# Kernel optimization log

Hardware: AMD Instinct MI355X
Metric: run time of the kernel (lower is better)

## Reference

```python
import jax, jax.numpy as jnp
import numpy as np

TOPK = 2


def setup_inputs() -> dict:
    key = jax.random.key(0)
    k0, k1, k2, k3, k4 = jax.random.split(key, 5)
    B, S, D, E, H = 4, 2048, 1024, 8, 2816
    return {
        "x": jax.random.normal(k0, (B, S, D), dtype=jnp.float32),
        "gate_w": jax.random.normal(k1, (E, D), dtype=jnp.float32) * 0.02,
        "w1": jax.random.normal(k2, (E, H, D), dtype=jnp.float32) * 0.02,
        "w2": jax.random.normal(k3, (E, D, H), dtype=jnp.float32) * 0.02,
        "w3": jax.random.normal(k4, (E, H, D), dtype=jnp.float32) * 0.02,
    }


def reference(x, gate_w, w1, w2, w3):
    B, S, D = x.shape
    E = gate_w.shape[0]
    T = B * S
    xf = x.reshape(T, D)

    # Router: top-k logits, softmax over the selected k, scatter into a
    # dense [T, E] combine-weight matrix (equivalent to the index_add combine).
    logits = xf @ gate_w.T                      # [T, E]
    tw, ti = jax.lax.top_k(logits, TOPK)        # [T, k]
    tw = jax.nn.softmax(tw, axis=-1)
    cw = jnp.zeros((T, E), dtype=xf.dtype).at[
        jnp.arange(T)[:, None], ti
    ].add(tw)                                   # [T, E] combine weights

    # Expert SwiGLU FFNs, combined with routing weights. Loop over the small
    # fixed expert count; tokens with cw==0 contribute zero, matching the
    # masked dispatch in the original module.
    out = jnp.zeros_like(xf)
    for e in range(E):
        h = jax.nn.silu(xf @ w1[e].T) * (xf @ w3[e].T)   # [T, H]
        out = out + cw[:, e:e + 1] * (h @ w2[e].T)       # [T, D]
    return out.reshape(B, S, D)
```

## Files before the change

### kernel.cpp

```cpp
#include <hip/hip_runtime.h>
#include <stdint.h>

#define T_TOK 8192
#define DIM   1024
#define NEXP  8
#define HID   2816

typedef __bf16 bf16x8 __attribute__((ext_vector_type(8)));
typedef float  f32x4  __attribute__((ext_vector_type(4)));

typedef __attribute__((address_space(3))) uint32_t lds_u32_t;
typedef __attribute__((address_space(1))) const uint32_t gbl_u32_t;

__device__ __forceinline__ void gl_lds16(const void* g, void* l) {
    __builtin_amdgcn_global_load_lds((gbl_u32_t*)g, (lds_u32_t*)l, 16, 0, 0);
}

__device__ __forceinline__ uint32_t f2bf_u(float f) {
    uint32_t u = __builtin_bit_cast(uint32_t, f);
    return u + 0x7fffu + ((u >> 16) & 1u);
}
__device__ __forceinline__ uint32_t pack2(float a, float b) {
    return (f2bf_u(a) >> 16) | (f2bf_u(b) & 0xffff0000u);
}


__global__ __launch_bounds__(256) void cvt_k(
    const float* __restrict__ s, unsigned short* __restrict__ d, int n8)
{
    int i = blockIdx.x * 256 + threadIdx.x;
    if (i < n8) {
        const float4* sp = (const float4*)(s + (size_t)i * 8);
        float4 a = sp[0], b = sp[1];
        uint4 o;
        o.x = pack2(a.x, a.y); o.y = pack2(a.z, a.w);
        o.z = pack2(b.x, b.y); o.w = pack2(b.z, b.w);
        ((uint4*)d)[i] = o;
    }
}

__global__ __launch_bounds__(256) void router_k(
    const float* __restrict__ x, const float* __restrict__ gw,
    int* __restrict__ cnt, int* __restrict__ slot_list,
    float* __restrict__ slot_w)
{
    const int wave = threadIdx.x >> 6, lane = threadIdx.x & 63;
    const int t = blockIdx.x * 4 + wave;
    const float4* xp = (const float4*)(x + (size_t)t * DIM + lane * 16);
    float4 xv[4];
#pragma unroll
    for (int i = 0; i < 4; ++i) xv[i] = xp[i];

    double lg[NEXP];
#pragma unroll
    for (int e = 0; e < NEXP; ++e) {
        const float4* gp = (const float4*)(gw + (size_t)e * DIM + lane * 16);
        double s = 0.0;
#pragma unroll
        for (int i = 0; i < 4; ++i) {
            float4 g = gp[i];
            s += (double)xv[i].x * g.x + (double)xv[i].y * g.y +
                 (double)xv[i].z * g.z + (double)xv[i].w * g.w;
        }
#pragma unroll
        for (int m = 32; m >= 1; m >>= 1) s += __shfl_xor(s, m, 64);
        lg[e] = s;
    }

    if (lane == 0) {
        int e0 = 0; double b0 = lg[0];
#pragma unroll
        for (int e = 1; e < NEXP; ++e)
            if (lg[e] > b0) { b0 = lg[e]; e0 = e; }
        int e1 = -1; double b1 = -1.0e300;
#pragma unroll
        for (int e = 0; e < NEXP; ++e)
            if (e != e0 && lg[e] > b1) { b1 = lg[e]; e1 = e; }

        float p0 = (float)(1.0 / (1.0 + exp(b1 - b0)));
        float p1 = 1.0f - p0;

        int pos0 = atomicAdd(&cnt[e0], 1);
        slot_list[e0 * T_TOK + pos0] = 2 * t;
        slot_w[2 * t] = p0;
        int pos1 = atomicAdd(&cnt[e1], 1);
        slot_list[e1 * T_TOK + pos1] = 2 * t + 1;
        slot_w[2 * t + 1] = p1;
    }
}

__global__ __launch_bounds__(256) void ffn1_k(
    const unsigned short* __restrict__ xb, const unsigned short* __restrict__ w1b,
    const unsigned short* __restrict__ w3b, const int* __restrict__ cnt,
    const int* __restrict__ slot_list, unsigned short* __restrict__ h_ws)
{
    __shared__ unsigned short As[128 * 32];
    __shared__ unsigned short B1s[64 * 32];
    __shared__ unsigned short B2s[64 * 32];
    __shared__ int slots_s[128];

    const int e = blockIdx.z;
    const int cntE = cnt[e];
    const int m0 = blockIdx.y * 128;
    if (m0 >= cntE) return;
    const int n0 = blockIdx.x * 64;
    const int tid = threadIdx.x;
    const int wave = tid >> 6, lane = tid & 63;

    if (tid < 128) {
        int idx = m0 + tid;
        slots_s[tid] = (idx < cntE) ? slot_list[e * T_TOK + idx] : -1;
    }
    __syncthreads();

    const int rr = lane >> 2;
    const int qsw = (lane & 3) ^ ((rr >> 1) & 3);
    const unsigned short* gsrc[4];
    unsigned short* ldst[4];
    if (wave < 2) {
#pragma unroll
        for (int i = 0; i < 4; ++i) {
            int row = wave * 64 + i * 16 + rr;
            int slot = slots_s[row];
            int tok = (slot >= 0) ? (slot >> 1) : 0;
            gsrc[i] = xb + (size_t)tok * DIM + qsw * 8;
            ldst[i] = &As[(wave * 64 + i * 16) * 32];
        }
    } else if (wave == 2) {
#pragma unroll
        for (int i = 0; i < 4; ++i) {
            int row = i * 16 + rr;
            gsrc[i] = w1b + ((size_t)e * HID + n0 + row) * DIM + qsw * 8;
            ldst[i] = &B1s[(i * 16) * 32];
        }
    } else {
#pragma unroll
        for (int i = 0; i < 4; ++i) {
            int row = i * 16 + rr;
            gsrc[i] = w3b + ((size_t)e * HID + n0 + row) * DIM + qsw * 8;
            ldst[i] = &B2s[(i * 16) * 32];
        }
    }

    const int wm = wave >> 1, wn = wave & 1;
    const int lrow = lane & 15, quad = lane >> 4;
    const int ksw = (quad ^ ((lrow >> 1) & 3)) * 8;

    f32x4 acc1[4][2], acc2[4][2];
    const f32x4 zf = {0.f, 0.f, 0.f, 0.f};
#pragma unroll
    for (int mi = 0; mi < 4; ++mi)
#pragma unroll
        for (int ni = 0; ni < 2; ++ni) { acc1[mi][ni] = zf; acc2[mi][ni] = zf; }

    for (int k0 = 0; k0 < DIM; k0 += 32) {
#pragma unroll
        for (int i = 0; i < 4; ++i) gl_lds16(gsrc[i], ldst[i]);
#pragma unroll
        for (int i = 0; i < 4; ++i) gsrc[i] += 32;
        __syncthreads();

        bf16x8 af[4], b1f[2], b2f[2];
#pragma unroll
        for (int mi = 0; mi < 4; ++mi)
            af[mi] = *(const bf16x8*)&As[(wm * 64 + mi * 16 + lrow) * 32 + ksw];
#pragma unroll
        for (int ni = 0; ni < 2; ++ni) {
            b1f[ni] = *(const bf16x8*)&B1s[(wn * 32 + ni * 16 + lrow) * 32 + ksw];
            b2f[ni] = *(const bf16x8*)&B2s[(wn * 32 + ni * 16 + lrow) * 32 + ksw];
        }
#pragma unroll
        for (int mi = 0; mi < 4; ++mi)
#pragma unroll
            for (int ni = 0; ni < 2; ++ni) {
                acc1[mi][ni] = __builtin_amdgcn_mfma_f32_16x16x32_bf16(
                    af[mi], b1f[ni], acc1[mi][ni], 0, 0, 0);
                acc2[mi][ni] = __builtin_amdgcn_mfma_f32_16x16x32_bf16(
                    af[mi], b2f[ni], acc2[mi][ni], 0, 0, 0);
            }
        __syncthreads();
    }

#pragma unroll
    for (int mi = 0; mi < 4; ++mi) {
#pragma unroll
        for (int r = 0; r < 4; ++r) {
            int mloc = wm * 64 + mi * 16 + quad * 4 + r;
            int slot = slots_s[mloc];
            if (slot >= 0) {
                unsigned short* hrow =
                    h_ws + (size_t)slot * HID + n0 + wn * 32 + lrow;
#pragma unroll
                for (int ni = 0; ni < 2; ++ni) {
                    float a1 = acc1[mi][ni][r], a3 = acc2[mi][ni][r];
                    float hv = (a1 / (1.f + __expf(-a1))) * a3;
                    hrow[ni * 16] = (unsigned short)(f2bf_u(hv) >> 16);
                }
            }
        }
    }
}

__global__ __launch_bounds__(256) void ffn2_k(
    const unsigned short* __restrict__ h_ws, const unsigned short* __restrict__ w2b,
    const int* __restrict__ cnt, const int* __restrict__ slot_list,
    const float* __restrict__ slot_w, float* __restrict__ out)
{
    __shared__ unsigned short As[128 * 32];
    __shared__ unsigned short Bs[128 * 32];
    __shared__ int slots_s[128];
    __shared__ float wgt_s[128];

    const int e = blockIdx.z;
    const int cntE = cnt[e];
    const int m0 = blockIdx.y * 128;
    if (m0 >= cntE) return;
    const int n0 = blockIdx.x * 128;
    const int tid = threadIdx.x;
    const int wave = tid >> 6, lane = tid & 63;

    if (tid < 128) {
        int idx = m0 + tid;
        int s = (idx < cntE) ? slot_list[e * T_TOK + idx] : -1;
        slots_s[tid] = s;
        wgt_s[tid] = (s >= 0) ? slot_w[s] : 0.f;
    }
    __syncthreads();

    const int rr = lane >> 2;
    const int qsw = (lane & 3) ^ ((rr >> 1) & 3);
    const unsigned short* gsrc[4];
    unsigned short* ldst[4];
    if (wave < 2) {
#pragma unroll
        for (int i = 0; i < 4; ++i) {
            int row = wave * 64 + i * 16 + rr;
            int slot = slots_s[row];
            int s = (slot >= 0) ? slot : 0;
            gsrc[i] = h_ws + (size_t)s * HID + qsw * 8;
            ldst[i] = &As[(wave * 64 + i * 16) * 32];
        }
    } else {
#pragma unroll
        for (int i = 0; i < 4; ++i) {
            int row = (wave - 2) * 64 + i * 16 + rr;
            gsrc[i] = w2b + ((size_t)e * DIM + n0 + row) * HID + qsw * 8;
            ldst[i] = &Bs[((wave - 2) * 64 + i * 16) * 32];
        }
    }

    const int wm = wave >> 1, wn = wave & 1;
    const int lrow = lane & 15, quad = lane >> 4;
    const int ksw = (quad ^ ((lrow >> 1) & 3)) * 8;

    f32x4 acc[4][4];
    const f32x4 zf = {0.f, 0.f, 0.f, 0.f};
#pragma unroll
    for (int mi = 0; mi < 4; ++mi)
#pragma unroll
        for (int ni = 0; ni < 4; ++ni) acc[mi][ni] = zf;

    for (int k0 = 0; k0 < HID; k0 += 32) {
#pragma unroll
        for (int i = 0; i < 4; ++i) gl_lds16(gsrc[i], ldst[i]);
#pragma unroll
        for (int i = 0; i < 4; ++i) gsrc[i] += 32;
        __syncthreads();

        bf16x8 af[4], bf[4];
#pragma unroll
        for (int mi = 0; mi < 4; ++mi)
            af[mi] = *(const bf16x8*)&As[(wm * 64 + mi * 16 + lrow) * 32 + ksw];
#pragma unroll
        for (int ni = 0; ni < 4; ++ni)
            bf[ni] = *(const bf16x8*)&Bs[(wn * 64 + ni * 16 + lrow) * 32 + ksw];
#pragma unroll
        for (int mi = 0; mi < 4; ++mi)
#pragma unroll
            for (int ni = 0; ni < 4; ++ni)
                acc[mi][ni] = __builtin_amdgcn_mfma_f32_16x16x32_bf16(
                    af[mi], bf[ni], acc[mi][ni], 0, 0, 0);
        __syncthreads();
    }

#pragma unroll
    for (int mi = 0; mi < 4; ++mi) {
#pragma unroll
        for (int r = 0; r < 4; ++r) {
            int mloc = wm * 64 + mi * 16 + quad * 4 + r;
            int slot = slots_s[mloc];
            if (slot >= 0) {
                int tok = slot >> 1;
                float w = wgt_s[mloc];
                float* orow = out + (size_t)tok * DIM + n0 + wn * 64 + lrow;
#pragma unroll
                for (int ni = 0; ni < 4; ++ni)
                    atomicAdd(&orow[ni * 16], acc[mi][ni][r] * w);
            }
        }
    }
}

extern "C" void kernel_launch(void* const* d_in, const int* in_sizes, int n_in,
                              void* d_out, int out_size, void* d_ws, size_t ws_size,
                              hipStream_t stream) {
    const float* x  = (const float*)d_in[0];
    const float* gw = (const float*)d_in[1];
    const float* w1 = (const float*)d_in[2];
    const float* w2 = (const float*)d_in[3];
    const float* w3 = (const float*)d_in[4];
    float* out = (float*)d_out;

    char* ws = (char*)d_ws;
    int*   cnt       = (int*)ws;
    int*   slot_list = (int*)(ws + 256);
    float* slot_w    = (float*)(ws + 256 + NEXP * T_TOK * 4);
    unsigned short* h_ws = (unsigned short*)(ws + 327936);
    unsigned short* x_bf = (unsigned short*)(ws + 92602624);
    unsigned short* w1_bf = (unsigned short*)(ws + 109379840);
    unsigned short* w3_bf = (unsigned short*)(ws + 155517184);
    unsigned short* w2_bf = (unsigned short*)(ws + 201654528);

    hipMemsetAsync(cnt, 0, 256, stream);
    hipMemsetAsync(out, 0, (size_t)T_TOK * DIM * sizeof(float), stream);

    const int nx = T_TOK * DIM / 8;
    const int nw = NEXP * HID * DIM / 8;
    cvt_k<<<(nx + 255) / 256, 256, 0, stream>>>(x, x_bf, nx);
    cvt_k<<<(nw + 255) / 256, 256, 0, stream>>>(w1, w1_bf, nw);
    cvt_k<<<(nw + 255) / 256, 256, 0, stream>>>(w3, w3_bf, nw);
    cvt_k<<<(nw + 255) / 256, 256, 0, stream>>>(w2, w2_bf, nw);

    router_k<<<T_TOK / 4, 256, 0, stream>>>(x, gw, cnt, slot_list, slot_w);
    ffn1_k<<<dim3(HID / 64, T_TOK / 128, NEXP), 256, 0, stream>>>(
        x_bf, w1_bf, w3_bf, cnt, slot_list, h_ws);
    ffn2_k<<<dim3(DIM / 128, T_TOK / 128, NEXP), 256, 0, stream>>>(
        h_ws, w2_bf, cnt, slot_list, slot_w, out);
}
```

Before: 929.4 us.

## Double-buffer LDS tiles in both expert GEMM kernels and raise MFMA priority

Both expert GEMM kernels (ffn1 and ffn2) now keep two LDS buffers per operand. Each iteration issues the global-to-LDS loads for the next K slice before running the MFMAs on the current slice, so memory latency overlaps with compute and only one barrier is needed per iteration instead of two. The MFMA block is also wrapped in s_setprio to favour issuing matrix instructions. The cost is double the LDS footprint per block, which may lower occupancy.

```diff
diff --git a/kernel.cpp b/kernel.cpp
--- a/kernel.cpp
+++ b/kernel.cpp
@@ -94,9 +94,9 @@
     const unsigned short* __restrict__ w3b, const int* __restrict__ cnt,
     const int* __restrict__ slot_list, unsigned short* __restrict__ h_ws)
 {
-    __shared__ unsigned short As[128 * 32];
-    __shared__ unsigned short B1s[64 * 32];
-    __shared__ unsigned short B2s[64 * 32];
+    __shared__ unsigned short As[2][128 * 32];
+    __shared__ unsigned short B1s[2][64 * 32];
+    __shared__ unsigned short B2s[2][64 * 32];
     __shared__ int slots_s[128];
 
     const int e = blockIdx.z;
@@ -117,28 +117,32 @@
     const int qsw = (lane & 3) ^ ((rr >> 1) & 3);
     const unsigned short* gsrc[4];
     unsigned short* ldst[4];
+    int bstride;
     if (wave < 2) {
+        bstride = 128 * 32;
 #pragma unroll
         for (int i = 0; i < 4; ++i) {
             int row = wave * 64 + i * 16 + rr;
             int slot = slots_s[row];
             int tok = (slot >= 0) ? (slot >> 1) : 0;
             gsrc[i] = xb + (size_t)tok * DIM + qsw * 8;
-            ldst[i] = &As[(wave * 64 + i * 16) * 32];
+            ldst[i] = &As[0][(wave * 64 + i * 16) * 32];
         }
     } else if (wave == 2) {
+        bstride = 64 * 32;
 #pragma unroll
         for (int i = 0; i < 4; ++i) {
             int row = i * 16 + rr;
             gsrc[i] = w1b + ((size_t)e * HID + n0 + row) * DIM + qsw * 8;
-            ldst[i] = &B1s[(i * 16) * 32];
+            ldst[i] = &B1s[0][(i * 16) * 32];
         }
     } else {
+        bstride = 64 * 32;
 #pragma unroll
         for (int i = 0; i < 4; ++i) {
             int row = i * 16 + rr;
             gsrc[i] = w3b + ((size_t)e * HID + n0 + row) * DIM + qsw * 8;
-            ldst[i] = &B2s[(i * 16) * 32];
+            ldst[i] = &B2s[0][(i * 16) * 32];
         }
     }
 
@@ -153,22 +157,36 @@
 #pragma unroll
         for (int ni = 0; ni < 2; ++ni) { acc1[mi][ni] = zf; acc2[mi][ni] = zf; }
 
-    for (int k0 = 0; k0 < DIM; k0 += 32) {
-#pragma unroll
-        for (int i = 0; i < 4; ++i) gl_lds16(gsrc[i], ldst[i]);
-#pragma unroll
-        for (int i = 0; i < 4; ++i) gsrc[i] += 32;
-        __syncthreads();
+    const int NST = DIM / 32;
+#pragma unroll
+    for (int i = 0; i < 4; ++i) gl_lds16(gsrc[i], ldst[i]);
+#pragma unroll
+    for (int i = 0; i < 4; ++i) gsrc[i] += 32;
+    __syncthreads();
+
+    for (int t = 0; t < NST; ++t) {
+        const int cur = t & 1, nxt = cur ^ 1;
+        if (t + 1 < NST) {
+#pragma unroll
+            for (int i = 0; i < 4; ++i)
+                gl_lds16(gsrc[i], ldst[i] + nxt * bstride);
+#pragma unroll
+            for (int i = 0; i < 4; ++i) gsrc[i] += 32;
+        }
+        const unsigned short* Ab  = &As[cur][0];
+        const unsigned short* B1b = &B1s[cur][0];
+        const unsigned short* B2b = &B2s[cur][0];
 
         bf16x8 af[4], b1f[2], b2f[2];
 #pragma unroll
         for (int mi = 0; mi < 4; ++mi)
-            af[mi] = *(const bf16x8*)&As[(wm * 64 + mi * 16 + lrow) * 32 + ksw];
+            af[mi] = *(const bf16x8*)&Ab[(wm * 64 + mi * 16 + lrow) * 32 + ksw];
 #pragma unroll
         for (int ni = 0; ni < 2; ++ni) {
-            b1f[ni] = *(const bf16x8*)&B1s[(wn * 32 + ni * 16 + lrow) * 32 + ksw];
-            b2f[ni] = *(const bf16x8*)&B2s[(wn * 32 + ni * 16 + lrow) * 32 + ksw];
-        }
+            b1f[ni] = *(const bf16x8*)&B1b[(wn * 32 + ni * 16 + lrow) * 32 + ksw];
+            b2f[ni] = *(const bf16x8*)&B2b[(wn * 32 + ni * 16 + lrow) * 32 + ksw];
+        }
+        __builtin_amdgcn_s_setprio(1);
 #pragma unroll
         for (int mi = 0; mi < 4; ++mi)
 #pragma unroll
@@ -178,7 +196,9 @@
                 acc2[mi][ni] = __builtin_amdgcn_mfma_f32_16x16x32_bf16(
                     af[mi], b2f[ni], acc2[mi][ni], 0, 0, 0);
             }
-        __syncthreads();
+        __builtin_amdgcn_s_setprio(0);
+
+        if (t + 1 < NST) __syncthreads();
     }
 
 #pragma unroll
@@ -206,8 +226,8 @@
     const int* __restrict__ cnt, const int* __restrict__ slot_list,
     const float* __restrict__ slot_w, float* __restrict__ out)
 {
-    __shared__ unsigned short As[128 * 32];
-    __shared__ unsigned short Bs[128 * 32];
+    __shared__ unsigned short As[2][128 * 32];
+    __shared__ unsigned short Bs[2][128 * 32];
     __shared__ int slots_s[128];
     __shared__ float wgt_s[128];
 
@@ -231,6 +251,7 @@
     const int qsw = (lane & 3) ^ ((rr >> 1) & 3);
     const unsigned short* gsrc[4];
     unsigned short* ldst[4];
+    const int bstride = 128 * 32;
     if (wave < 2) {
 #pragma unroll
         for (int i = 0; i < 4; ++i) {
@@ -238,14 +259,14 @@
             int slot = slots_s[row];
             int s = (slot >= 0) ? slot : 0;
             gsrc[i] = h_ws + (size_t)s * HID + qsw * 8;
-            ldst[i] = &As[(wave * 64 + i * 16) * 32];
+            ldst[i] = &As[0][(wave * 64 + i * 16) * 32];
         }
     } else {
 #pragma unroll
         for (int i = 0; i < 4; ++i) {
             int row = (wave - 2) * 64 + i * 16 + rr;
             gsrc[i] = w2b + ((size_t)e * DIM + n0 + row) * HID + qsw * 8;
-            ldst[i] = &Bs[((wave - 2) * 64 + i * 16) * 32];
+            ldst[i] = &Bs[0][((wave - 2) * 64 + i * 16) * 32];
         }
     }
 
@@ -260,27 +281,42 @@
 #pragma unroll
         for (int ni = 0; ni < 4; ++ni) acc[mi][ni] = zf;
 
-    for (int k0 = 0; k0 < HID; k0 += 32) {
-#pragma unroll
-        for (int i = 0; i < 4; ++i) gl_lds16(gsrc[i], ldst[i]);
-#pragma unroll
-        for (int i = 0; i < 4; ++i) gsrc[i] += 32;
-        __syncthreads();
+    const int NST = HID / 32;
+#pragma unroll
+    for (int i = 0; i < 4; ++i) gl_lds16(gsrc[i], ldst[i]);
+#pragma unroll
+    for (int i = 0; i < 4; ++i) gsrc[i] += 32;
+    __syncthreads();
+
+    for (int t = 0; t < NST; ++t) {
+        const int cur = t & 1, nxt = cur ^ 1;
+        if (t + 1 < NST) {
+#pragma unroll
+            for (int i = 0; i < 4; ++i)
+                gl_lds16(gsrc[i], ldst[i] + nxt * bstride);
+#pragma unroll
+            for (int i = 0; i < 4; ++i) gsrc[i] += 32;
+        }
+        const unsigned short* Ab = &As[cur][0];
+        const unsigned short* Bb = &Bs[cur][0];
 
         bf16x8 af[4], bf[4];
 #pragma unroll
         for (int mi = 0; mi < 4; ++mi)
-            af[mi] = *(const bf16x8*)&As[(wm * 64 + mi * 16 + lrow) * 32 + ksw];
+            af[mi] = *(const bf16x8*)&Ab[(wm * 64 + mi * 16 + lrow) * 32 + ksw];
 #pragma unroll
         for (int ni = 0; ni < 4; ++ni)
-            bf[ni] = *(const bf16x8*)&Bs[(wn * 64 + ni * 16 + lrow) * 32 + ksw];
+            bf[ni] = *(const bf16x8*)&Bb[(wn * 64 + ni * 16 + lrow) * 32 + ksw];
+        __builtin_amdgcn_s_setprio(1);
 #pragma unroll
         for (int mi = 0; mi < 4; ++mi)
 #pragma unroll
             for (int ni = 0; ni < 4; ++ni)
                 acc[mi][ni] = __builtin_amdgcn_mfma_f32_16x16x32_bf16(
                     af[mi], bf[ni], acc[mi][ni], 0, 0, 0);
-        __syncthreads();
+        __builtin_amdgcn_s_setprio(0);
+
+        if (t + 1 < NST) __syncthreads();
     }
 
 #pragma unroll
```

After: 941.0 us. No clear change (+1.2%).

## Double-buffer activation tiles in LDS and load weights directly into registers

Applied to the files above, without the earlier changes.

Both expert GEMM kernels now stage only the gathered activation rows in LDS, using a two-stage ping-pong buffer. Weight fragments are loaded straight from global memory into registers, also double-buffered, so the next K-step loads overlap the current MFMAs, and s_setprio is raised around the MFMA bursts. This aims to hide global load latency and drop one of the two barriers per K-step. In exchange, each wave fetches its own weight fragments with no reuse across the waves that share the same columns, which uses more registers and global bandwidth.

```diff
diff --git a/kernel.cpp b/kernel.cpp
--- a/kernel.cpp
+++ b/kernel.cpp
@@ -94,9 +94,7 @@
     const unsigned short* __restrict__ w3b, const int* __restrict__ cnt,
     const int* __restrict__ slot_list, unsigned short* __restrict__ h_ws)
 {
-    __shared__ unsigned short As[128 * 32];
-    __shared__ unsigned short B1s[64 * 32];
-    __shared__ unsigned short B2s[64 * 32];
+    __shared__ unsigned short As[2][128 * 32];
     __shared__ int slots_s[128];
 
     const int e = blockIdx.z;
@@ -115,37 +113,27 @@
 
     const int rr = lane >> 2;
     const int qsw = (lane & 3) ^ ((rr >> 1) & 3);
-    const unsigned short* gsrc[4];
-    unsigned short* ldst[4];
-    if (wave < 2) {
-#pragma unroll
-        for (int i = 0; i < 4; ++i) {
-            int row = wave * 64 + i * 16 + rr;
-            int slot = slots_s[row];
-            int tok = (slot >= 0) ? (slot >> 1) : 0;
-            gsrc[i] = xb + (size_t)tok * DIM + qsw * 8;
-            ldst[i] = &As[(wave * 64 + i * 16) * 32];
-        }
-    } else if (wave == 2) {
-#pragma unroll
-        for (int i = 0; i < 4; ++i) {
-            int row = i * 16 + rr;
-            gsrc[i] = w1b + ((size_t)e * HID + n0 + row) * DIM + qsw * 8;
-            ldst[i] = &B1s[(i * 16) * 32];
-        }
-    } else {
-#pragma unroll
-        for (int i = 0; i < 4; ++i) {
-            int row = i * 16 + rr;
-            gsrc[i] = w3b + ((size_t)e * HID + n0 + row) * DIM + qsw * 8;
-            ldst[i] = &B2s[(i * 16) * 32];
-        }
+    const unsigned short* gsrc[2];
+    unsigned short* ldst[2];
+    const int bstride = 128 * 32;
+#pragma unroll
+    for (int i = 0; i < 2; ++i) {
+        int row = wave * 32 + i * 16 + rr;
+        int slot = slots_s[row];
+        int tok = (slot >= 0) ? (slot >> 1) : 0;
+        gsrc[i] = xb + (size_t)tok * DIM + qsw * 8;
+        ldst[i] = &As[0][(wave * 32 + i * 16) * 32];
     }
 
     const int wm = wave >> 1, wn = wave & 1;
     const int lrow = lane & 15, quad = lane >> 4;
     const int ksw = (quad ^ ((lrow >> 1) & 3)) * 8;
 
+    const unsigned short* w1p =
+        w1b + ((size_t)e * HID + n0 + wn * 32 + lrow) * DIM + quad * 8;
+    const unsigned short* w3p =
+        w3b + ((size_t)e * HID + n0 + wn * 32 + lrow) * DIM + quad * 8;
+
     f32x4 acc1[4][2], acc2[4][2];
     const f32x4 zf = {0.f, 0.f, 0.f, 0.f};
 #pragma unroll
@@ -153,32 +141,85 @@
 #pragma unroll
         for (int ni = 0; ni < 2; ++ni) { acc1[mi][ni] = zf; acc2[mi][ni] = zf; }
 
-    for (int k0 = 0; k0 < DIM; k0 += 32) {
-#pragma unroll
-        for (int i = 0; i < 4; ++i) gl_lds16(gsrc[i], ldst[i]);
-#pragma unroll
-        for (int i = 0; i < 4; ++i) gsrc[i] += 32;
-        __syncthreads();
-
-        bf16x8 af[4], b1f[2], b2f[2];
-#pragma unroll
-        for (int mi = 0; mi < 4; ++mi)
-            af[mi] = *(const bf16x8*)&As[(wm * 64 + mi * 16 + lrow) * 32 + ksw];
-#pragma unroll
-        for (int ni = 0; ni < 2; ++ni) {
-            b1f[ni] = *(const bf16x8*)&B1s[(wn * 32 + ni * 16 + lrow) * 32 + ksw];
-            b2f[ni] = *(const bf16x8*)&B2s[(wn * 32 + ni * 16 + lrow) * 32 + ksw];
-        }
-#pragma unroll
-        for (int mi = 0; mi < 4; ++mi)
-#pragma unroll
-            for (int ni = 0; ni < 2; ++ni) {
-                acc1[mi][ni] = __builtin_amdgcn_mfma_f32_16x16x32_bf16(
-                    af[mi], b1f[ni], acc1[mi][ni], 0, 0, 0);
-                acc2[mi][ni] = __builtin_amdgcn_mfma_f32_16x16x32_bf16(
-                    af[mi], b2f[ni], acc2[mi][ni], 0, 0, 0);
-            }
-        __syncthreads();
+    const int NST = DIM / 32;
+
+    bf16x8 bA10, bA11, bA30, bA31;
+    bf16x8 bB10, bB11, bB30, bB31;
+
+#pragma unroll
+    for (int i = 0; i < 2; ++i) { gl_lds16(gsrc[i], ldst[i]); gsrc[i] += 32; }
+    bA10 = *(const bf16x8*)(w1p);
+    bA11 = *(const bf16x8*)(w1p + 16 * DIM);
+    bA30 = *(const bf16x8*)(w3p);
+    bA31 = *(const bf16x8*)(w3p + 16 * DIM);
+    w1p += 32; w3p += 32;
+    __syncthreads();
+
+    for (int t = 0; t < NST; t += 2) {
+        {
+#pragma unroll
+            for (int i = 0; i < 2; ++i) {
+                gl_lds16(gsrc[i], ldst[i] + bstride); gsrc[i] += 32;
+            }
+            bB10 = *(const bf16x8*)(w1p);
+            bB11 = *(const bf16x8*)(w1p + 16 * DIM);
+            bB30 = *(const bf16x8*)(w3p);
+            bB31 = *(const bf16x8*)(w3p + 16 * DIM);
+            w1p += 32; w3p += 32;
+
+            const unsigned short* Ab = &As[0][0];
+            bf16x8 af[4];
+#pragma unroll
+            for (int mi = 0; mi < 4; ++mi)
+                af[mi] = *(const bf16x8*)&Ab[(wm * 64 + mi * 16 + lrow) * 32 + ksw];
+            __builtin_amdgcn_s_setprio(1);
+#pragma unroll
+            for (int mi = 0; mi < 4; ++mi) {
+                acc1[mi][0] = __builtin_amdgcn_mfma_f32_16x16x32_bf16(
+                    af[mi], bA10, acc1[mi][0], 0, 0, 0);
+                acc1[mi][1] = __builtin_amdgcn_mfma_f32_16x16x32_bf16(
+                    af[mi], bA11, acc1[mi][1], 0, 0, 0);
+                acc2[mi][0] = __builtin_amdgcn_mfma_f32_16x16x32_bf16(
+                    af[mi], bA30, acc2[mi][0], 0, 0, 0);
+                acc2[mi][1] = __builtin_amdgcn_mfma_f32_16x16x32_bf16(
+                    af[mi], bA31, acc2[mi][1], 0, 0, 0);
+            }
+            __builtin_amdgcn_s_setprio(0);
+            __syncthreads();
+        }
+        {
+            const bool more = (t + 2 < NST);
+            if (more) {
+#pragma unroll
+                for (int i = 0; i < 2; ++i) {
+                    gl_lds16(gsrc[i], ldst[i]); gsrc[i] += 32;
+                }
+                bA10 = *(const bf16x8*)(w1p);
+                bA11 = *(const bf16x8*)(w1p + 16 * DIM);
+                bA30 = *(const bf16x8*)(w3p);
+                bA31 = *(const bf16x8*)(w3p + 16 * DIM);
+                w1p += 32; w3p += 32;
+            }
+            const unsigned short* Ab = &As[1][0];
+            bf16x8 af[4];
+#pragma unroll
+            for (int mi = 0; mi < 4; ++mi)
+                af[mi] = *(const bf16x8*)&Ab[(wm * 64 + mi * 16 + lrow) * 32 + ksw];
+            __builtin_amdgcn_s_setprio(1);
+#pragma unroll
+            for (int mi = 0; mi < 4; ++mi) {
+                acc1[mi][0] = __builtin_amdgcn_mfma_f32_16x16x32_bf16(
+                    af[mi], bB10, acc1[mi][0], 0, 0, 0);
+                acc1[mi][1] = __builtin_amdgcn_mfma_f32_16x16x32_bf16(
+                    af[mi], bB11, acc1[mi][1], 0, 0, 0);
+                acc2[mi][0] = __builtin_amdgcn_mfma_f32_16x16x32_bf16(
+                    af[mi], bB30, acc2[mi][0], 0, 0, 0);
+                acc2[mi][1] = __builtin_amdgcn_mfma_f32_16x16x32_bf16(
+                    af[mi], bB31, acc2[mi][1], 0, 0, 0);
+            }
+            __builtin_amdgcn_s_setprio(0);
+            if (more) __syncthreads();
+        }
     }
 
 #pragma unroll
@@ -206,8 +247,7 @@
     const int* __restrict__ cnt, const int* __restrict__ slot_list,
     const float* __restrict__ slot_w, float* __restrict__ out)
 {
-    __shared__ unsigned short As[128 * 32];
-    __shared__ unsigned short Bs[128 * 32];
+    __shared__ unsigned short As[2][128 * 32];
     __shared__ int slots_s[128];
     __shared__ float wgt_s[128];
 
@@ -229,30 +269,25 @@
 
     const int rr = lane >> 2;
     const int qsw = (lane & 3) ^ ((rr >> 1) & 3);
-    const unsigned short* gsrc[4];
-    unsigned short* ldst[4];
-    if (wave < 2) {
-#pragma unroll
-        for (int i = 0; i < 4; ++i) {
-            int row = wave * 64 + i * 16 + rr;
-            int slot = slots_s[row];
-            int s = (slot >= 0) ? slot : 0;
-            gsrc[i] = h_ws + (size_t)s * HID + qsw * 8;
-            ldst[i] = &As[(wave * 64 + i * 16) * 32];
-        }
-    } else {
-#pragma unroll
-        for (int i = 0; i < 4; ++i) {
-            int row = (wave - 2) * 64 + i * 16 + rr;
-            gsrc[i] = w2b + ((size_t)e * DIM + n0 + row) * HID + qsw * 8;
-            ldst[i] = &Bs[((wave - 2) * 64 + i * 16) * 32];
-        }
+    const unsigned short* gsrc[2];
+    unsigned short* ldst[2];
+    const int bstride = 128 * 32;
+#pragma unroll
+    for (int i = 0; i < 2; ++i) {
+        int row = wave * 32 + i * 16 + rr;
+        int slot = slots_s[row];
+        int s = (slot >= 0) ? slot : 0;
+        gsrc[i] = h_ws + (size_t)s * HID + qsw * 8;
+        ldst[i] = &As[0][(wave * 32 + i * 16) * 32];
     }
 
     const int wm = wave >> 1, wn = wave & 1;
     const int lrow = lane & 15, quad = lane >> 4;
     const int ksw = (quad ^ ((lrow >> 1) & 3)) * 8;
 
+    const unsigned short* w2p =
+        w2b + ((size_t)e * DIM + n0 + wn * 64 + lrow) * HID + quad * 8;
+
     f32x4 acc[4][4];
     const f32x4 zf = {0.f, 0.f, 0.f, 0.f};
 #pragma unroll
@@ -260,27 +295,85 @@
 #pragma unroll
         for (int ni = 0; ni < 4; ++ni) acc[mi][ni] = zf;
 
-    for (int k0 = 0; k0 < HID; k0 += 32) {
-#pragma unroll
-        for (int i = 0; i < 4; ++i) gl_lds16(gsrc[i], ldst[i]);
-#pragma unroll
-        for (int i = 0; i < 4; ++i) gsrc[i] += 32;
-        __syncthreads();
-
-        bf16x8 af[4], bf[4];
-#pragma unroll
-        for (int mi = 0; mi < 4; ++mi)
-            af[mi] = *(const bf16x8*)&As[(wm * 64 + mi * 16 + lrow) * 32 + ksw];
-#pragma unroll
-        for (int ni = 0; ni < 4; ++ni)
-            bf[ni] = *(const bf16x8*)&Bs[(wn * 64 + ni * 16 + lrow) * 32 + ksw];
-#pragma unroll
-        for (int mi = 0; mi < 4; ++mi)
-#pragma unroll
-            for (int ni = 0; ni < 4; ++ni)
-                acc[mi][ni] = __builtin_amdgcn_mfma_f32_16x16x32_bf16(
-                    af[mi], bf[ni], acc[mi][ni], 0, 0, 0);
-        __syncthreads();
+    const int NST = HID / 32;
+
+    bf16x8 bA0, bA1, bA2, bA3;
+    bf16x8 bB0, bB1, bB2, bB3;
+
+#pragma unroll
+    for (int i = 0; i < 2; ++i) { gl_lds16(gsrc[i], ldst[i]); gsrc[i] += 32; }
+    bA0 = *(const bf16x8*)(w2p);
+    bA1 = *(const bf16x8*)(w2p + 16 * HID);
+    bA2 = *(const bf16x8*)(w2p + 32 * HID);
+    bA3 = *(const bf16x8*)(w2p + 48 * HID);
+    w2p += 32;
+    __syncthreads();
+
+    for (int t = 0; t < NST; t += 2) {
+        {
+#pragma unroll
+            for (int i = 0; i < 2; ++i) {
+                gl_lds16(gsrc[i], ldst[i] + bstride); gsrc[i] += 32;
+            }
+            bB0 = *(const bf16x8*)(w2p);
+            bB1 = *(const bf16x8*)(w2p + 16 * HID);
+            bB2 = *(const bf16x8*)(w2p + 32 * HID);
+            bB3 = *(const bf16x8*)(w2p + 48 * HID);
+            w2p += 32;
+
+            const unsigned short* Ab = &As[0][0];
+            bf16x8 af[4];
+#pragma unroll
+            for (int mi = 0; mi < 4; ++mi)
+                af[mi] = *(const bf16x8*)&Ab[(wm * 64 + mi * 16 + lrow) * 32 + ksw];
+            __builtin_amdgcn_s_setprio(1);
+#pragma unroll
+            for (int mi = 0; mi < 4; ++mi) {
+                acc[mi][0] = __builtin_amdgcn_mfma_f32_16x16x32_bf16(
+                    af[mi], bA0, acc[mi][0], 0, 0, 0);
+                acc[mi][1] = __builtin_amdgcn_mfma_f32_16x16x32_bf16(
+                    af[mi], bA1, acc[mi][1], 0, 0, 0);
+                acc[mi][2] = __builtin_amdgcn_mfma_f32_16x16x32_bf16(
+                    af[mi], bA2, acc[mi][2], 0, 0, 0);
+                acc[mi][3] = __builtin_amdgcn_mfma_f32_16x16x32_bf16(
+                    af[mi], bA3, acc[mi][3], 0, 0, 0);
+            }
+            __builtin_amdgcn_s_setprio(0);
+            __syncthreads();
+        }
+        {
+            const bool more = (t + 2 < NST);
+            if (more) {
+#pragma unroll
+                for (int i = 0; i < 2; ++i) {
+                    gl_lds16(gsrc[i], ldst[i]); gsrc[i] += 32;
+                }
+                bA0 = *(const bf16x8*)(w2p);
+                bA1 = *(const bf16x8*)(w2p + 16 * HID);
+                bA2 = *(const bf16x8*)(w2p + 32 * HID);
+                bA3 = *(const bf16x8*)(w2p + 48 * HID);
+                w2p += 32;
+            }
+            const unsigned short* Ab = &As[1][0];
+            bf16x8 af[4];
+#pragma unroll
+            for (int mi = 0; mi < 4; ++mi)
+                af[mi] = *(const bf16x8*)&Ab[(wm * 64 + mi * 16 + lrow) * 32 + ksw];
+            __builtin_amdgcn_s_setprio(1);
+#pragma unroll
+            for (int mi = 0; mi < 4; ++mi) {
+                acc[mi][0] = __builtin_amdgcn_mfma_f32_16x16x32_bf16(
+                    af[mi], bB0, acc[mi][0], 0, 0, 0);
+                acc[mi][1] = __builtin_amdgcn_mfma_f32_16x16x32_bf16(
+                    af[mi], bB1, acc[mi][1], 0, 0, 0);
+                acc[mi][2] = __builtin_amdgcn_mfma_f32_16x16x32_bf16(
+                    af[mi], bB2, acc[mi][2], 0, 0, 0);
+                acc[mi][3] = __builtin_amdgcn_mfma_f32_16x16x32_bf16(
+                    af[mi], bB3, acc[mi][3], 0, 0, 0);
+            }
+            __builtin_amdgcn_s_setprio(0);
+            if (more) __syncthreads();
+        }
     }
 
 #pragma unroll
```

New measurement: 1.301 ms. 1.4x slower.

## Triple-buffer FFN GEMM loads and replace atomic combine with per-slot output pass

Applied to the files above, without the earlier changes.

Both expert GEMM kernels now use a three-stage LDS ring with async global-to-LDS loads, a partial vmcnt wait plus one barrier per step, and raised wave priority around the MFMA block, so memory loads overlap compute. The second GEMM writes weighted per-slot results to a workspace instead of doing atomic adds into the output. A new combine kernel sums each token's two slots, which also drops the output memset. This costs triple LDS per block, which may lower occupancy, and adds an extra pass over a large fp32 buffer that reuses the x_bf workspace region after it is consumed.

```diff
diff --git a/kernel.cpp b/kernel.cpp
--- a/kernel.cpp
+++ b/kernel.cpp
@@ -24,6 +24,11 @@
     return (f2bf_u(a) >> 16) | (f2bf_u(b) & 0xffff0000u);
 }
 
+
+#define WAIT4 do { asm volatile("s_waitcnt vmcnt(4)" ::: "memory"); \
+    __builtin_amdgcn_s_barrier(); __builtin_amdgcn_sched_barrier(0); } while (0)
+#define WAIT0 do { asm volatile("s_waitcnt vmcnt(0)" ::: "memory"); \
+    __builtin_amdgcn_s_barrier(); __builtin_amdgcn_sched_barrier(0); } while (0)
 
 __global__ __launch_bounds__(256) void cvt_k(
     const float* __restrict__ s, unsigned short* __restrict__ d, int n8)
@@ -94,9 +99,9 @@
     const unsigned short* __restrict__ w3b, const int* __restrict__ cnt,
     const int* __restrict__ slot_list, unsigned short* __restrict__ h_ws)
 {
-    __shared__ unsigned short As[128 * 32];
-    __shared__ unsigned short B1s[64 * 32];
-    __shared__ unsigned short B2s[64 * 32];
+    __shared__ unsigned short As[3][128 * 32];
+    __shared__ unsigned short B1s[3][64 * 32];
+    __shared__ unsigned short B2s[3][64 * 32];
     __shared__ int slots_s[128];
 
     const int e = blockIdx.z;
@@ -116,7 +121,7 @@
     const int rr = lane >> 2;
     const int qsw = (lane & 3) ^ ((rr >> 1) & 3);
     const unsigned short* gsrc[4];
-    unsigned short* ldst[4];
+    unsigned short *l0[4], *l1[4], *l2[4];
     if (wave < 2) {
 #pragma unroll
         for (int i = 0; i < 4; ++i) {
@@ -124,21 +129,27 @@
             int slot = slots_s[row];
             int tok = (slot >= 0) ? (slot >> 1) : 0;
             gsrc[i] = xb + (size_t)tok * DIM + qsw * 8;
-            ldst[i] = &As[(wave * 64 + i * 16) * 32];
+            l0[i] = &As[0][(wave * 64 + i * 16) * 32];
+            l1[i] = &As[1][(wave * 64 + i * 16) * 32];
+            l2[i] = &As[2][(wave * 64 + i * 16) * 32];
         }
     } else if (wave == 2) {
 #pragma unroll
         for (int i = 0; i < 4; ++i) {
             int row = i * 16 + rr;
             gsrc[i] = w1b + ((size_t)e * HID + n0 + row) * DIM + qsw * 8;
-            ldst[i] = &B1s[(i * 16) * 32];
+            l0[i] = &B1s[0][(i * 16) * 32];
+            l1[i] = &B1s[1][(i * 16) * 32];
+            l2[i] = &B1s[2][(i * 16) * 32];
         }
     } else {
 #pragma unroll
         for (int i = 0; i < 4; ++i) {
             int row = i * 16 + rr;
             gsrc[i] = w3b + ((size_t)e * HID + n0 + row) * DIM + qsw * 8;
-            ldst[i] = &B2s[(i * 16) * 32];
+            l0[i] = &B2s[0][(i * 16) * 32];
+            l1[i] = &B2s[1][(i * 16) * 32];
+            l2[i] = &B2s[2][(i * 16) * 32];
         }
     }
 
@@ -153,33 +164,45 @@
 #pragma unroll
         for (int ni = 0; ni < 2; ++ni) { acc1[mi][ni] = zf; acc2[mi][ni] = zf; }
 
-    for (int k0 = 0; k0 < DIM; k0 += 32) {
-#pragma unroll
-        for (int i = 0; i < 4; ++i) gl_lds16(gsrc[i], ldst[i]);
-#pragma unroll
-        for (int i = 0; i < 4; ++i) gsrc[i] += 32;
-        __syncthreads();
-
-        bf16x8 af[4], b1f[2], b2f[2];
-#pragma unroll
-        for (int mi = 0; mi < 4; ++mi)
-            af[mi] = *(const bf16x8*)&As[(wm * 64 + mi * 16 + lrow) * 32 + ksw];
-#pragma unroll
-        for (int ni = 0; ni < 2; ++ni) {
-            b1f[ni] = *(const bf16x8*)&B1s[(wn * 32 + ni * 16 + lrow) * 32 + ksw];
-            b2f[ni] = *(const bf16x8*)&B2s[(wn * 32 + ni * 16 + lrow) * 32 + ksw];
-        }
-#pragma unroll
-        for (int mi = 0; mi < 4; ++mi)
-#pragma unroll
-            for (int ni = 0; ni < 2; ++ni) {
-                acc1[mi][ni] = __builtin_amdgcn_mfma_f32_16x16x32_bf16(
-                    af[mi], b1f[ni], acc1[mi][ni], 0, 0, 0);
-                acc2[mi][ni] = __builtin_amdgcn_mfma_f32_16x16x32_bf16(
-                    af[mi], b2f[ni], acc2[mi][ni], 0, 0, 0);
-            }
-        __syncthreads();
-    }
+#define FFN1_STG(N) do { \
+    gl_lds16(gsrc[0], l##N[0]); gl_lds16(gsrc[1], l##N[1]); \
+    gl_lds16(gsrc[2], l##N[2]); gl_lds16(gsrc[3], l##N[3]); \
+    gsrc[0] += 32; gsrc[1] += 32; gsrc[2] += 32; gsrc[3] += 32; } while (0)
+
+#define FFN1_COMP(N) do { \
+    bf16x8 af[4], b1f[2], b2f[2]; \
+    _Pragma("unroll") \
+    for (int mi = 0; mi < 4; ++mi) \
+        af[mi] = *(const bf16x8*)&As[N][(wm * 64 + mi * 16 + lrow) * 32 + ksw]; \
+    _Pragma("unroll") \
+    for (int ni = 0; ni < 2; ++ni) { \
+        b1f[ni] = *(const bf16x8*)&B1s[N][(wn * 32 + ni * 16 + lrow) * 32 + ksw]; \
+        b2f[ni] = *(const bf16x8*)&B2s[N][(wn * 32 + ni * 16 + lrow) * 32 + ksw]; \
+    } \
+    __builtin_amdgcn_s_setprio(1); \
+    _Pragma("unroll") \
+    for (int mi = 0; mi < 4; ++mi) { \
+        acc1[mi][0] = __builtin_amdgcn_mfma_f32_16x16x32_bf16(af[mi], b1f[0], acc1[mi][0], 0, 0, 0); \
+        acc1[mi][1] = __builtin_amdgcn_mfma_f32_16x16x32_bf16(af[mi], b1f[1], acc1[mi][1], 0, 0, 0); \
+        acc2[mi][0] = __builtin_amdgcn_mfma_f32_16x16x32_bf16(af[mi], b2f[0], acc2[mi][0], 0, 0, 0); \
+        acc2[mi][1] = __builtin_amdgcn_mfma_f32_16x16x32_bf16(af[mi], b2f[1], acc2[mi][1], 0, 0, 0); \
+    } \
+    __builtin_amdgcn_s_setprio(0); } while (0)
+
+    FFN1_STG(0);
+    FFN1_STG(1);
+    WAIT4;
+
+    for (int g = 0; g < 10; ++g) {
+        FFN1_STG(2); FFN1_COMP(0); WAIT4;
+        FFN1_STG(0); FFN1_COMP(1); WAIT4;
+        FFN1_STG(1); FFN1_COMP(2); WAIT4;
+    }
+    FFN1_COMP(0); WAIT0;
+    FFN1_COMP(1);
+
+#undef FFN1_STG
+#undef FFN1_COMP
 
 #pragma unroll
     for (int mi = 0; mi < 4; ++mi) {
@@ -204,10 +227,10 @@
 __global__ __launch_bounds__(256) void ffn2_k(
     const unsigned short* __restrict__ h_ws, const unsigned short* __restrict__ w2b,
     const int* __restrict__ cnt, const int* __restrict__ slot_list,
-    const float* __restrict__ slot_w, float* __restrict__ out)
-{
-    __shared__ unsigned short As[128 * 32];
-    __shared__ unsigned short Bs[128 * 32];
+    const float* __restrict__ slot_w, float* __restrict__ y_ws)
+{
+    __shared__ unsigned short As[3][128 * 32];
+    __shared__ unsigned short Bs[3][128 * 32];
     __shared__ int slots_s[128];
     __shared__ float wgt_s[128];
 
@@ -230,7 +253,7 @@
     const int rr = lane >> 2;
     const int qsw = (lane & 3) ^ ((rr >> 1) & 3);
     const unsigned short* gsrc[4];
-    unsigned short* ldst[4];
+    unsigned short *l0[4], *l1[4], *l2[4];
     if (wave < 2) {
 #pragma unroll
         for (int i = 0; i < 4; ++i) {
@@ -238,14 +261,18 @@
             int slot = slots_s[row];
             int s = (slot >= 0) ? slot : 0;
             gsrc[i] = h_ws + (size_t)s * HID + qsw * 8;
-            ldst[i] = &As[(wave * 64 + i * 16) * 32];
+            l0[i] = &As[0][(wave * 64 + i * 16) * 32];
+            l1[i] = &As[1][(wave * 64 + i * 16) * 32];
+            l2[i] = &As[2][(wave * 64 + i * 16) * 32];
         }
     } else {
 #pragma unroll
         for (int i = 0; i < 4; ++i) {
             int row = (wave - 2) * 64 + i * 16 + rr;
             gsrc[i] = w2b + ((size_t)e * DIM + n0 + row) * HID + qsw * 8;
-            ldst[i] = &Bs[((wave - 2) * 64 + i * 16) * 32];
+            l0[i] = &Bs[0][((wave - 2) * 64 + i * 16) * 32];
+            l1[i] = &Bs[1][((wave - 2) * 64 + i * 16) * 32];
+            l2[i] = &Bs[2][((wave - 2) * 64 + i * 16) * 32];
         }
     }
 
@@ -260,28 +287,45 @@
 #pragma unroll
         for (int ni = 0; ni < 4; ++ni) acc[mi][ni] = zf;
 
-    for (int k0 = 0; k0 < HID; k0 += 32) {
-#pragma unroll
-        for (int i = 0; i < 4; ++i) gl_lds16(gsrc[i], ldst[i]);
-#pragma unroll
-        for (int i = 0; i < 4; ++i) gsrc[i] += 32;
-        __syncthreads();
-
-        bf16x8 af[4], bf[4];
-#pragma unroll
-        for (int mi = 0; mi < 4; ++mi)
-            af[mi] = *(const bf16x8*)&As[(wm * 64 + mi * 16 + lrow) * 32 + ksw];
-#pragma unroll
-        for (int ni = 0; ni < 4; ++ni)
-            bf[ni] = *(const bf16x8*)&Bs[(wn * 64 + ni * 16 + lrow) * 32 + ksw];
-#pragma unroll
-        for (int mi = 0; mi < 4; ++mi)
-#pragma unroll
-            for (int ni = 0; ni < 4; ++ni)
-                acc[mi][ni] = __builtin_amdgcn_mfma_f32_16x16x32_bf16(
-                    af[mi], bf[ni], acc[mi][ni], 0, 0, 0);
-        __syncthreads();
-    }
+#define FFN2_STG(N) do { \
+    gl_lds16(gsrc[0], l##N[0]); gl_lds16(gsrc[1], l##N[1]); \
+    gl_lds16(gsrc[2], l##N[2]); gl_lds16(gsrc[3], l##N[3]); \
+    gsrc[0] += 32; gsrc[1] += 32; gsrc[2] += 32; gsrc[3] += 32; } while (0)
+
+#define FFN2_COMP(N) do { \
+    bf16x8 af[4], bf[4]; \
+    _Pragma("unroll") \
+    for (int mi = 0; mi < 4; ++mi) \
+        af[mi] = *(const bf16x8*)&As[N][(wm * 64 + mi * 16 + lrow) * 32 + ksw]; \
+    _Pragma("unroll") \
+    for (int ni = 0; ni < 4; ++ni) \
+        bf[ni] = *(const bf16x8*)&Bs[N][(wn * 64 + ni * 16 + lrow) * 32 + ksw]; \
+    __builtin_amdgcn_s_setprio(1); \
+    _Pragma("unroll") \
+    for (int mi = 0; mi < 4; ++mi) { \
+        acc[mi][0] = __builtin_amdgcn_mfma_f32_16x16x32_bf16(af[mi], bf[0], acc[mi][0], 0, 0, 0); \
+        acc[mi][1] = __builtin_amdgcn_mfma_f32_16x16x32_bf16(af[mi], bf[1], acc[mi][1], 0, 0, 0); \
+        acc[mi][2] = __builtin_amdgcn_mfma_f32_16x16x32_bf16(af[mi], bf[2], acc[mi][2], 0, 0, 0); \
+        acc[mi][3] = __builtin_amdgcn_mfma_f32_16x16x32_bf16(af[mi], bf[3], acc[mi][3], 0, 0, 0); \
+    } \
+    __builtin_amdgcn_s_setprio(0); } while (0)
+
+    FFN2_STG(0);
+    FFN2_STG(1);
+    WAIT4;
+
+    for (int g = 0; g < 28; ++g) {
+        FFN2_STG(2); FFN2_COMP(0); WAIT4;
+        FFN2_STG(0); FFN2_COMP(1); WAIT4;
+        FFN2_STG(1); FFN2_COMP(2); WAIT4;
+    }
+    FFN2_STG(2); FFN2_COMP(0); WAIT4;
+    FFN2_STG(0); FFN2_COMP(1); WAIT4;
+    FFN2_COMP(2); WAIT0;
+    FFN2_COMP(0);
+
+#undef FFN2_STG
+#undef FFN2_COMP
 
 #pragma unroll
     for (int mi = 0; mi < 4; ++mi) {
@@ -290,15 +334,26 @@
             int mloc = wm * 64 + mi * 16 + quad * 4 + r;
             int slot = slots_s[mloc];
             if (slot >= 0) {
-                int tok = slot >> 1;
                 float w = wgt_s[mloc];
-                float* orow = out + (size_t)tok * DIM + n0 + wn * 64 + lrow;
+                float* yrow = y_ws + (size_t)slot * DIM + n0 + wn * 64 + lrow;
 #pragma unroll
                 for (int ni = 0; ni < 4; ++ni)
-                    atomicAdd(&orow[ni * 16], acc[mi][ni][r] * w);
+                    yrow[ni * 16] = acc[mi][ni][r] * w;
             }
         }
     }
+}
+
+__global__ __launch_bounds__(256) void combine_k(
+    const float* __restrict__ y, float* __restrict__ out)
+{
+    int i = blockIdx.x * 256 + threadIdx.x;
+    int t = i >> 8, d = i & 255;
+    const float4* a = (const float4*)(y + (size_t)(2 * t) * DIM) + d;
+    const float4* b = (const float4*)(y + (size_t)(2 * t + 1) * DIM) + d;
+    float4 va = *a, vb = *b;
+    float4 o = {va.x + vb.x, va.y + vb.y, va.z + vb.z, va.w + vb.w};
+    ((float4*)(out + (size_t)t * DIM))[d] = o;
 }
 
 extern "C" void kernel_launch(void* const* d_in, const int* in_sizes, int n_in,
@@ -320,9 +375,9 @@
     unsigned short* w1_bf = (unsigned short*)(ws + 109379840);
     unsigned short* w3_bf = (unsigned short*)(ws + 155517184);
     unsigned short* w2_bf = (unsigned short*)(ws + 201654528);
+    float* y_ws = (float*)(ws + 92602624);
 
     hipMemsetAsync(cnt, 0, 256, stream);
-    hipMemsetAsync(out, 0, (size_t)T_TOK * DIM * sizeof(float), stream);
 
     const int nx = T_TOK * DIM / 8;
     const int nw = NEXP * HID * DIM / 8;
@@ -335,5 +390,6 @@
     ffn1_k<<<dim3(HID / 64, T_TOK / 128, NEXP), 256, 0, stream>>>(
         x_bf, w1_bf, w3_bf, cnt, slot_list, h_ws);
     ffn2_k<<<dim3(DIM / 128, T_TOK / 128, NEXP), 256, 0, stream>>>(
-        h_ws, w2_bf, cnt, slot_list, slot_w, out);
-}
+        h_ws, w2_bf, cnt, slot_list, slot_w, y_ws);
+    combine_k<<<T_TOK, 256, 0, stream>>>(y_ws, out);
+}
```

New measurement: 899.3 us. 3.2% less time.
